# Optimization experiments

Measured on AMD Instinct MI355X. Metric: run time of the kernel, lower is better.

The kernel has to match this reference:

```python
import jax, jax.numpy as jnp
import numpy as np

HIDDEN = 512


def setup_inputs() -> dict:
    key = jax.random.key(0)
    k1, k2, k3, k4, k5 = jax.random.split(key, 5)
    scale = 1.0 / np.sqrt(HIDDEN)
    return {
        "decoder_hidden": jax.random.normal(k1, (64, HIDDEN), dtype=jnp.float32),
        "encoder_outputs": jax.random.normal(k2, (4096, 64, HIDDEN), dtype=jnp.float32),
        "W1": jax.random.uniform(k3, (HIDDEN, HIDDEN), jnp.float32, -scale, scale),
        "W2": jax.random.uniform(k4, (HIDDEN, HIDDEN), jnp.float32, -scale, scale),
        "v": jax.random.uniform(k5, (HIDDEN,), jnp.float32, -scale, scale),
    }


def reference(decoder_hidden, encoder_outputs, W1, W2, v):
    # decoder_hidden: (B, H); encoder_outputs: (S, B, H)
    enc = jnp.transpose(encoder_outputs, (1, 0, 2))          # (B, S, H)
    dec_proj = decoder_hidden @ W1.T                          # (B, H) — no need to repeat over S
    enc_proj = jnp.einsum('bsh,gh->bsg', enc, W2)             # (B, S, H)
    energy = jnp.tanh(dec_proj[:, None, :] + enc_proj) @ v    # (B, S)
    attn_weights = jax.nn.softmax(energy, axis=1)             # (B, S)
    context = jnp.einsum('bs,bsh->bh', attn_weights, enc)     # (B, H)
    return (context, attn_weights)
```

## Files before the change

### kernel.cpp

```cpp
#include <hip/hip_runtime.h>
#include <math.h>


#define BATCH 64
#define SEQ   4096
#define HID   512

typedef __attribute__((ext_vector_type(8))) short bf16x8;
typedef __attribute__((ext_vector_type(4))) float f32x4;

__device__ __forceinline__ float fast_tanh(float x) {
    return 1.0f - 2.0f / (__expf(2.0f * x) + 1.0f);
}

__device__ __forceinline__ unsigned cvt2(float lo, float hi) {
    unsigned r;
    asm("v_cvt_pk_bf16_f32 %0, %1, %2" : "=v"(r) : "v"(lo), "v"(hi));
    return r;
}

__device__ __forceinline__ void gload_lds16(const void* g, void* l) {
    __builtin_amdgcn_global_load_lds(
        (const __attribute__((address_space(1))) unsigned*)g,
        (__attribute__((address_space(3))) unsigned*)l, 16, 0, 0);
}

__global__ void k_cvtW2(const float* __restrict__ W2, ushort* __restrict__ W2t)
{
    const int n  = blockIdx.x * 256 + threadIdx.x;
    const int kb = n >> 11;
    const int f  = n & 2047;
    const int g  = f >> 2, rg = f & 3;
    const float* src = W2 + (size_t)g * HID + kb * 32 + rg * 8;
    const float4 x = *reinterpret_cast<const float4*>(src);
    const float4 y = *reinterpret_cast<const float4*>(src + 4);
    uint4 u;
    u.x = cvt2(x.x, x.y);  u.y = cvt2(x.z, x.w);
    u.z = cvt2(y.x, y.y);  u.w = cvt2(y.z, y.w);
    const int slot = f ^ ((f >> 3) & 7);
    *reinterpret_cast<uint4*>(W2t + (size_t)kb * 16384 + slot * 8) = u;
}

__global__ void k_decproj(const float* __restrict__ dh,
                          const float* __restrict__ W1,
                          float* __restrict__ dp)
{
    __shared__ float wrow[HID];
    const int g = blockIdx.x;
    const int t = threadIdx.x;
    for (int i = t; i < HID; i += 256) wrow[i] = W1[g * HID + i];
    __syncthreads();

    const int b = t >> 2, q = t & 3;
    const float* dhb = dh + b * HID + q * 128;
    const float* wr  = wrow + q * 128;
    float acc = 0.f;
    #pragma unroll 8
    for (int i = 0; i < 128; i += 4) {
        const float4 d4 = *reinterpret_cast<const float4*>(dhb + i);
        acc = fmaf(d4.x, wr[i + 0], acc);
        acc = fmaf(d4.y, wr[i + 1], acc);
        acc = fmaf(d4.z, wr[i + 2], acc);
        acc = fmaf(d4.w, wr[i + 3], acc);
    }
    acc += __shfl_xor(acc, 1);
    acc += __shfl_xor(acc, 2);
    if (q == 0) dp[b * HID + g] = acc;
}

#define LDA 40

__global__ __launch_bounds__(512, 2)
void k_energy(const float* __restrict__ enc, const ushort* __restrict__ W2t,
              const float* __restrict__ dp,  const float* __restrict__ v,
              float* __restrict__ energy)
{
    __shared__ __align__(16) ushort As[128 * LDA];
    __shared__ __align__(16) ushort Bs[2][16384];
    __shared__ float part[8][64];

    const int b    = blockIdx.y;
    const int s0   = blockIdx.x * 128;
    const int t    = threadIdx.x;
    const int lane = t & 63;
    const int wv   = t >> 6;
    const int wm   = wv >> 2, wn = wv & 3;
    const int gl   = lane & 15, rg = lane >> 4;

    f32x4 acc[4][8];
    const f32x4 z = {0.f, 0.f, 0.f, 0.f};
    #pragma unroll
    for (int m = 0; m < 4; ++m)
        #pragma unroll
        for (int n = 0; n < 8; ++n) acc[m][n] = z;

    const int arow = t >> 2, akq = t & 3;
    const float* aptr = enc + ((size_t)(s0 + arow) * BATCH + b) * HID + akq * 8;

    int aoff[4];
    #pragma unroll
    for (int m = 0; m < 4; ++m)
        aoff[m] = (wm * 64 + m * 16 + gl) * LDA + rg * 8;
    int boff[8];
    #pragma unroll
    for (int n = 0; n < 8; ++n) {
        const int g = wn * 128 + n * 16 + gl;
        const int f = g * 4 + rg;
        boff[n] = (f ^ ((f >> 3) & 7)) * 8;
    }

    const char* wsrc = (const char*)W2t;
    #pragma unroll
    for (int r = 0; r < 4; ++r)
        gload_lds16(wsrc + (r * 512 + t) * 16, (char*)&Bs[0][0] + (r * 512 + t) * 16);
    float4 a0 = *reinterpret_cast<const float4*>(aptr);
    float4 a1 = *reinterpret_cast<const float4*>(aptr + 4);

    for (int kb = 0; kb < 16; ++kb) {
        __syncthreads();
        {
            uint4 aw;
            aw.x = cvt2(a0.x, a0.y);  aw.y = cvt2(a0.z, a0.w);
            aw.z = cvt2(a1.x, a1.y);  aw.w = cvt2(a1.z, a1.w);
            *reinterpret_cast<uint4*>(&As[arow * LDA + akq * 8]) = aw;
        }
        __syncthreads();

        const int cur = kb & 1;
        if (kb < 15) {
            const char* src = wsrc + (size_t)(kb + 1) * 32768;
            #pragma unroll
            for (int r = 0; r < 4; ++r)
                gload_lds16(src + (r * 512 + t) * 16,
                            (char*)&Bs[cur ^ 1][0] + (r * 512 + t) * 16);
            a0 = *reinterpret_cast<const float4*>(aptr + (kb + 1) * 32);
            a1 = *reinterpret_cast<const float4*>(aptr + (kb + 1) * 32 + 4);
        }

        bf16x8 af[4], bf[8];
        #pragma unroll
        for (int m = 0; m < 4; ++m)
            af[m] = *reinterpret_cast<const bf16x8*>(&As[aoff[m]]);
        #pragma unroll
        for (int n = 0; n < 8; ++n)
            bf[n] = *reinterpret_cast<const bf16x8*>(&Bs[cur][boff[n]]);
        #pragma unroll
        for (int m = 0; m < 4; ++m)
            #pragma unroll
            for (int n = 0; n < 8; ++n)
                acc[m][n] = __builtin_amdgcn_mfma_f32_16x16x32_bf16(
                    af[m], bf[n], acc[m][n], 0, 0, 0);
    }

    float dpv[8], vv[8];
    #pragma unroll
    for (int n = 0; n < 8; ++n) {
        const int g = wn * 128 + n * 16 + gl;
        dpv[n] = dp[b * HID + g];
        vv[n]  = v[g];
    }
    float p[4][4];
    #pragma unroll
    for (int m = 0; m < 4; ++m)
        #pragma unroll
        for (int r = 0; r < 4; ++r) p[m][r] = 0.f;
    #pragma unroll
    for (int n = 0; n < 8; ++n)
        #pragma unroll
        for (int m = 0; m < 4; ++m)
            #pragma unroll
            for (int r = 0; r < 4; ++r)
                p[m][r] += fast_tanh(dpv[n] + acc[m][n][r]) * vv[n];

    #pragma unroll
    for (int m = 0; m < 4; ++m)
        #pragma unroll
        for (int r = 0; r < 4; ++r) {
            float x = p[m][r];
            x += __shfl_xor(x, 1);
            x += __shfl_xor(x, 2);
            x += __shfl_xor(x, 4);
            x += __shfl_xor(x, 8);
            p[m][r] = x;
        }
    if (gl == 0) {
        #pragma unroll
        for (int m = 0; m < 4; ++m)
            #pragma unroll
            for (int r = 0; r < 4; ++r)
                part[wv][m * 16 + rg * 4 + r] = p[m][r];
    }
    __syncthreads();

    if (t < 128) {
        const int row = t & 63, wmf = t >> 6;
        const float e = part[wmf * 4 + 0][row] + part[wmf * 4 + 1][row]
                      + part[wmf * 4 + 2][row] + part[wmf * 4 + 3][row];
        energy[(size_t)b * SEQ + s0 + t] = e;
    }
}

__global__ void k_softmax(float* __restrict__ attn)
{
    __shared__ float redm[4], reds[4];
    const int b = blockIdx.x, t = threadIdx.x;
    float* e = attn + (size_t)b * SEQ;

    float4 ev[4];
    float m = -3.4e38f;
    #pragma unroll
    for (int i = 0; i < 4; ++i) {
        ev[i] = *reinterpret_cast<const float4*>(e + i * 1024 + t * 4);
        m = fmaxf(m, fmaxf(fmaxf(ev[i].x, ev[i].y), fmaxf(ev[i].z, ev[i].w)));
    }
    #pragma unroll
    for (int off = 1; off < 64; off <<= 1) m = fmaxf(m, __shfl_xor(m, off));
    if ((t & 63) == 0) redm[t >> 6] = m;
    __syncthreads();
    m = fmaxf(fmaxf(redm[0], redm[1]), fmaxf(redm[2], redm[3]));

    float s = 0.f;
    #pragma unroll
    for (int i = 0; i < 4; ++i) {
        ev[i].x = __expf(ev[i].x - m);  ev[i].y = __expf(ev[i].y - m);
        ev[i].z = __expf(ev[i].z - m);  ev[i].w = __expf(ev[i].w - m);
        s += (ev[i].x + ev[i].y) + (ev[i].z + ev[i].w);
    }
    #pragma unroll
    for (int off = 1; off < 64; off <<= 1) s += __shfl_xor(s, off);
    if ((t & 63) == 0) reds[t >> 6] = s;
    __syncthreads();
    s = (reds[0] + reds[1]) + (reds[2] + reds[3]);
    const float inv = 1.0f / s;

    #pragma unroll
    for (int i = 0; i < 4; ++i) {
        const float4 w4 = make_float4(ev[i].x * inv, ev[i].y * inv,
                                      ev[i].z * inv, ev[i].w * inv);
        *reinterpret_cast<float4*>(e + i * 1024 + t * 4) = w4;
    }
}

__global__ void k_ctxpart(const float* __restrict__ enc,
                          const float* __restrict__ attn,
                          float* __restrict__ pctx)
{
    __shared__ float w[256];
    const int b  = blockIdx.x;
    const int sp = blockIdx.y;
    const int t  = threadIdx.x;

    w[t] = attn[(size_t)b * SEQ + sp * 256 + t];
    __syncthreads();

    const float2* e2 = reinterpret_cast<const float2*>(enc);
    size_t idx = ((size_t)sp * 256 * BATCH + b) * (HID / 2) + t;
    const size_t stride = (size_t)BATCH * (HID / 2);

    float ax = 0.f, ay = 0.f;
    #pragma unroll 4
    for (int s = 0; s < 256; ++s) {
        const float2 ev = e2[idx];
        const float ws = w[s];
        ax = fmaf(ws, ev.x, ax);
        ay = fmaf(ws, ev.y, ay);
        idx += stride;
    }
    float2* p2 = reinterpret_cast<float2*>(pctx);
    p2[((size_t)sp * BATCH + b) * (HID / 2) + t] = make_float2(ax, ay);
}

__global__ void k_ctxsum(const float* __restrict__ pctx,
                         float* __restrict__ ctx)
{
    const int i = blockIdx.x * 256 + threadIdx.x;
    float s = 0.f;
    #pragma unroll
    for (int sp = 0; sp < 16; ++sp) s += pctx[(size_t)sp * BATCH * HID + i];
    ctx[i] = s;
}

extern "C" void kernel_launch(void* const* d_in, const int* in_sizes, int n_in,
                              void* d_out, int out_size, void* d_ws, size_t ws_size,
                              hipStream_t stream)
{
    const float* dh  = (const float*)d_in[0];
    const float* enc = (const float*)d_in[1];
    const float* W1  = (const float*)d_in[2];
    const float* W2  = (const float*)d_in[3];
    const float* v   = (const float*)d_in[4];

    float* out  = (float*)d_out;
    float* ctx  = out;
    float* attn = out + BATCH * HID;

    float*  dp   = (float*)d_ws;
    ushort* W2t  = (ushort*)(dp + BATCH * HID);
    float*  pctx = (float*)(W2t + HID * HID);

    k_cvtW2  <<<128, 256, 0, stream>>>(W2, W2t);
    k_decproj<<<HID, 256, 0, stream>>>(dh, W1, dp);
    k_energy <<<dim3(SEQ / 128, BATCH), 512, 0, stream>>>(enc, W2t, dp, v, attn);
    k_softmax<<<BATCH, 256, 0, stream>>>(attn);
    k_ctxpart<<<dim3(BATCH, 16), 256, 0, stream>>>(enc, attn, pctx);
    k_ctxsum <<<BATCH * HID / 256, 256, 0, stream>>>(pctx, ctx);
}
```

Baseline: 394.0 us.

## Deepen A-tile register prefetch and replace syncthreads with fine-grained waitcnt barriers

The main GEMM loop now prefetches encoder rows two k-blocks ahead using a triple-buffered register array instead of one ahead. The __syncthreads calls are replaced by explicit s_waitcnt vmcnt/lgkmcnt plus raw s_barrier, and B-fragment LDS reads are issued before the second barrier. The aim is to hide global load latency and cut full-drain synchronization stalls. The manual vmcnt counts depend on exact load ordering, and the extra prefetch registers raise register pressure, which could hurt occupancy.

```diff
diff --git a/kernel.cpp b/kernel.cpp
--- a/kernel.cpp
+++ b/kernel.cpp
@@ -110,40 +110,55 @@
     }
 
     const char* wsrc = (const char*)W2t;
+    float4 ar[3][2];
+
+    ar[0][0] = *reinterpret_cast<const float4*>(aptr);
+    ar[0][1] = *reinterpret_cast<const float4*>(aptr + 4);
     #pragma unroll
     for (int r = 0; r < 4; ++r)
-        gload_lds16(wsrc + (r * 512 + t) * 16, (char*)&Bs[0][0] + (r * 512 + t) * 16);
-    float4 a0 = *reinterpret_cast<const float4*>(aptr);
-    float4 a1 = *reinterpret_cast<const float4*>(aptr + 4);
-
+        gload_lds16(wsrc + (r * 512 + t) * 16,
+                    (char*)&Bs[0][0] + (r * 512 + t) * 16);
+    ar[1][0] = *reinterpret_cast<const float4*>(aptr + 32);
+    ar[1][1] = *reinterpret_cast<const float4*>(aptr + 36);
+
+    #pragma unroll
     for (int kb = 0; kb < 16; ++kb) {
-        __syncthreads();
+        if (kb < 15) asm volatile("s_waitcnt vmcnt(2)" ::: "memory");
+        else         asm volatile("s_waitcnt vmcnt(0)" ::: "memory");
+        __builtin_amdgcn_s_barrier();
+
         {
             uint4 aw;
+            const float4 a0 = ar[kb % 3][0], a1 = ar[kb % 3][1];
             aw.x = cvt2(a0.x, a0.y);  aw.y = cvt2(a0.z, a0.w);
             aw.z = cvt2(a1.x, a1.y);  aw.w = cvt2(a1.z, a1.w);
             *reinterpret_cast<uint4*>(&As[arow * LDA + akq * 8]) = aw;
         }
-        __syncthreads();
-
-        const int cur = kb & 1;
+        bf16x8 bf[8];
+        #pragma unroll
+        for (int n = 0; n < 8; ++n)
+            bf[n] = *reinterpret_cast<const bf16x8*>(&Bs[kb & 1][boff[n]]);
+
+        asm volatile("s_waitcnt lgkmcnt(0)" ::: "memory");
+        __builtin_amdgcn_s_barrier();
+
+        bf16x8 af[4];
+        #pragma unroll
+        for (int m = 0; m < 4; ++m)
+            af[m] = *reinterpret_cast<const bf16x8*>(&As[aoff[m]]);
+
         if (kb < 15) {
             const char* src = wsrc + (size_t)(kb + 1) * 32768;
             #pragma unroll
             for (int r = 0; r < 4; ++r)
                 gload_lds16(src + (r * 512 + t) * 16,
-                            (char*)&Bs[cur ^ 1][0] + (r * 512 + t) * 16);
-            a0 = *reinterpret_cast<const float4*>(aptr + (kb + 1) * 32);
-            a1 = *reinterpret_cast<const float4*>(aptr + (kb + 1) * 32 + 4);
+                            (char*)&Bs[(kb + 1) & 1][0] + (r * 512 + t) * 16);
         }
-
-        bf16x8 af[4], bf[8];
-        #pragma unroll
-        for (int m = 0; m < 4; ++m)
-            af[m] = *reinterpret_cast<const bf16x8*>(&As[aoff[m]]);
-        #pragma unroll
-        for (int n = 0; n < 8; ++n)
-            bf[n] = *reinterpret_cast<const bf16x8*>(&Bs[cur][boff[n]]);
+        if (kb < 14) {
+            ar[(kb + 2) % 3][0] = *reinterpret_cast<const float4*>(aptr + (kb + 2) * 32);
+            ar[(kb + 2) % 3][1] = *reinterpret_cast<const float4*>(aptr + (kb + 2) * 32 + 4);
+        }
+
         #pragma unroll
         for (int m = 0; m < 4; ++m)
             #pragma unroll
```

Result: slower. 414.9 us (+5.3%).

## Split energy GEMM across output-column halves with smaller tiles and partial energies

Applied to the files above, without the earlier changes.

The energy kernel now uses 64-row sequence tiles and 256-wide output-column halves per block, with 256 threads and a higher occupancy target. Each half writes a partial energy that the softmax kernel sums, and blocks are ordered so the two halves of the same encoder tile run close together. The aim is more parallelism and smaller per-block register and LDS footprint, so more waves can hide latency. The cost is that each encoder tile is loaded and converted twice (ideally served from L2) and an extra partial-energy buffer is read back.

```diff
diff --git a/kernel.cpp b/kernel.cpp
--- a/kernel.cpp
+++ b/kernel.cpp
@@ -70,29 +70,34 @@
 
 #define LDA 40
 
-__global__ __launch_bounds__(512, 2)
+__global__ __launch_bounds__(256, 3)
 void k_energy(const float* __restrict__ enc, const ushort* __restrict__ W2t,
               const float* __restrict__ dp,  const float* __restrict__ v,
-              float* __restrict__ energy)
-{
-    __shared__ __align__(16) ushort As[128 * LDA];
-    __shared__ __align__(16) ushort Bs[2][16384];
-    __shared__ float part[8][64];
-
-    const int b    = blockIdx.y;
-    const int s0   = blockIdx.x * 128;
+              float* __restrict__ eparts)
+{
+    __shared__ __align__(16) ushort As[64 * LDA];
+    __shared__ __align__(16) ushort Bs[2][8192];
+    __shared__ float part[4][64];
+
+    const int idx  = blockIdx.x;
+    const int g16  = idx >> 4, rr = idx & 15;
+    const int gh   = rr >> 3;
+    const int pair = (g16 << 3) | (rr & 7);
+    const int schunk = pair & 63;
+    const int b      = pair >> 6;
+    const int s0     = schunk * 64;
+
     const int t    = threadIdx.x;
     const int lane = t & 63;
     const int wv   = t >> 6;
-    const int wm   = wv >> 2, wn = wv & 3;
     const int gl   = lane & 15, rg = lane >> 4;
 
-    f32x4 acc[4][8];
+    f32x4 acc[4][4];
     const f32x4 z = {0.f, 0.f, 0.f, 0.f};
     #pragma unroll
     for (int m = 0; m < 4; ++m)
         #pragma unroll
-        for (int n = 0; n < 8; ++n) acc[m][n] = z;
+        for (int n = 0; n < 4; ++n) acc[m][n] = z;
 
     const int arow = t >> 2, akq = t & 3;
     const float* aptr = enc + ((size_t)(s0 + arow) * BATCH + b) * HID + akq * 8;
@@ -100,22 +105,24 @@
     int aoff[4];
     #pragma unroll
     for (int m = 0; m < 4; ++m)
-        aoff[m] = (wm * 64 + m * 16 + gl) * LDA + rg * 8;
-    int boff[8];
-    #pragma unroll
-    for (int n = 0; n < 8; ++n) {
-        const int g = wn * 128 + n * 16 + gl;
-        const int f = g * 4 + rg;
-        boff[n] = (f ^ ((f >> 3) & 7)) * 8;
-    }
-
-    const char* wsrc = (const char*)W2t;
-    #pragma unroll
-    for (int r = 0; r < 4; ++r)
-        gload_lds16(wsrc + (r * 512 + t) * 16, (char*)&Bs[0][0] + (r * 512 + t) * 16);
+        aoff[m] = (m * 16 + gl) * LDA + rg * 8;
+    int boff[4];
+    #pragma unroll
+    for (int n = 0; n < 4; ++n) {
+        const int fl = (wv * 64 + n * 16 + gl) * 4 + rg;
+        boff[n] = (fl ^ ((fl >> 3) & 7)) * 8;
+    }
+
+    const char* wsrc = (const char*)W2t + gh * 16384;
+
+    #pragma unroll
+    for (int q = 0; q < 4; ++q)
+        gload_lds16(wsrc + (q * 256 + t) * 16,
+                    (char*)&Bs[0][0] + (q * 256 + t) * 16);
     float4 a0 = *reinterpret_cast<const float4*>(aptr);
     float4 a1 = *reinterpret_cast<const float4*>(aptr + 4);
 
+    #pragma unroll
     for (int kb = 0; kb < 16; ++kb) {
         __syncthreads();
         {
@@ -126,36 +133,35 @@
         }
         __syncthreads();
 
-        const int cur = kb & 1;
         if (kb < 15) {
             const char* src = wsrc + (size_t)(kb + 1) * 32768;
             #pragma unroll
-            for (int r = 0; r < 4; ++r)
-                gload_lds16(src + (r * 512 + t) * 16,
-                            (char*)&Bs[cur ^ 1][0] + (r * 512 + t) * 16);
+            for (int q = 0; q < 4; ++q)
+                gload_lds16(src + (q * 256 + t) * 16,
+                            (char*)&Bs[(kb + 1) & 1][0] + (q * 256 + t) * 16);
             a0 = *reinterpret_cast<const float4*>(aptr + (kb + 1) * 32);
             a1 = *reinterpret_cast<const float4*>(aptr + (kb + 1) * 32 + 4);
         }
 
-        bf16x8 af[4], bf[8];
+        bf16x8 af[4], bfr[4];
         #pragma unroll
         for (int m = 0; m < 4; ++m)
             af[m] = *reinterpret_cast<const bf16x8*>(&As[aoff[m]]);
         #pragma unroll
-        for (int n = 0; n < 8; ++n)
-            bf[n] = *reinterpret_cast<const bf16x8*>(&Bs[cur][boff[n]]);
+        for (int n = 0; n < 4; ++n)
+            bfr[n] = *reinterpret_cast<const bf16x8*>(&Bs[kb & 1][boff[n]]);
         #pragma unroll
         for (int m = 0; m < 4; ++m)
             #pragma unroll
-            for (int n = 0; n < 8; ++n)
+            for (int n = 0; n < 4; ++n)
                 acc[m][n] = __builtin_amdgcn_mfma_f32_16x16x32_bf16(
-                    af[m], bf[n], acc[m][n], 0, 0, 0);
-    }
-
-    float dpv[8], vv[8];
-    #pragma unroll
-    for (int n = 0; n < 8; ++n) {
-        const int g = wn * 128 + n * 16 + gl;
+                    af[m], bfr[n], acc[m][n], 0, 0, 0);
+    }
+
+    float dpv[4], vv[4];
+    #pragma unroll
+    for (int n = 0; n < 4; ++n) {
+        const int g = gh * 256 + wv * 64 + n * 16 + gl;
         dpv[n] = dp[b * HID + g];
         vv[n]  = v[g];
     }
@@ -165,7 +171,7 @@
         #pragma unroll
         for (int r = 0; r < 4; ++r) p[m][r] = 0.f;
     #pragma unroll
-    for (int n = 0; n < 8; ++n)
+    for (int n = 0; n < 4; ++n)
         #pragma unroll
         for (int m = 0; m < 4; ++m)
             #pragma unroll
@@ -192,25 +198,27 @@
     }
     __syncthreads();
 
-    if (t < 128) {
-        const int row = t & 63, wmf = t >> 6;
-        const float e = part[wmf * 4 + 0][row] + part[wmf * 4 + 1][row]
-                      + part[wmf * 4 + 2][row] + part[wmf * 4 + 3][row];
-        energy[(size_t)b * SEQ + s0 + t] = e;
-    }
-}
-
-__global__ void k_softmax(float* __restrict__ attn)
+    if (t < 64) {
+        const float e = part[0][t] + part[1][t] + part[2][t] + part[3][t];
+        eparts[(size_t)gh * BATCH * SEQ + (size_t)b * SEQ + s0 + t] = e;
+    }
+}
+
+__global__ void k_softmax(const float* __restrict__ eparts,
+                          float* __restrict__ attn)
 {
     __shared__ float redm[4], reds[4];
     const int b = blockIdx.x, t = threadIdx.x;
-    float* e = attn + (size_t)b * SEQ;
+    const float* e0 = eparts + (size_t)b * SEQ;
+    const float* e1 = eparts + (size_t)BATCH * SEQ + (size_t)b * SEQ;
 
     float4 ev[4];
     float m = -3.4e38f;
     #pragma unroll
     for (int i = 0; i < 4; ++i) {
-        ev[i] = *reinterpret_cast<const float4*>(e + i * 1024 + t * 4);
+        const float4 x = *reinterpret_cast<const float4*>(e0 + i * 1024 + t * 4);
+        const float4 y = *reinterpret_cast<const float4*>(e1 + i * 1024 + t * 4);
+        ev[i] = make_float4(x.x + y.x, x.y + y.y, x.z + y.z, x.w + y.w);
         m = fmaxf(m, fmaxf(fmaxf(ev[i].x, ev[i].y), fmaxf(ev[i].z, ev[i].w)));
     }
     #pragma unroll
@@ -233,11 +241,12 @@
     s = (reds[0] + reds[1]) + (reds[2] + reds[3]);
     const float inv = 1.0f / s;
 
+    float* o = attn + (size_t)b * SEQ;
     #pragma unroll
     for (int i = 0; i < 4; ++i) {
         const float4 w4 = make_float4(ev[i].x * inv, ev[i].y * inv,
                                       ev[i].z * inv, ev[i].w * inv);
-        *reinterpret_cast<float4*>(e + i * 1024 + t * 4) = w4;
+        *reinterpret_cast<float4*>(o + i * 1024 + t * 4) = w4;
     }
 }
 
@@ -294,14 +303,16 @@
     float* ctx  = out;
     float* attn = out + BATCH * HID;
 
-    float*  dp   = (float*)d_ws;
-    ushort* W2t  = (ushort*)(dp + BATCH * HID);
-    float*  pctx = (float*)(W2t + HID * HID);
+    float*  dp      = (float*)d_ws;
+    ushort* W2t     = (ushort*)(dp + BATCH * HID);
+    float*  shared2 = (float*)(W2t + HID * HID);
+    float*  eparts  = shared2;
+    float*  pctx    = shared2;
 
     k_cvtW2  <<<128, 256, 0, stream>>>(W2, W2t);
     k_decproj<<<HID, 256, 0, stream>>>(dh, W1, dp);
-    k_energy <<<dim3(SEQ / 128, BATCH), 512, 0, stream>>>(enc, W2t, dp, v, attn);
-    k_softmax<<<BATCH, 256, 0, stream>>>(attn);
+    k_energy <<<8192, 256, 0, stream>>>(enc, W2t, dp, v, eparts);
+    k_softmax<<<BATCH, 256, 0, stream>>>(eparts, attn);
     k_ctxpart<<<dim3(BATCH, 16), 256, 0, stream>>>(enc, attn, pctx);
     k_ctxsum <<<BATCH * HID / 256, 256, 0, stream>>>(pctx, ctx);
 }
```

Measured after the change: 371.1 us. -5.8%, faster.
